# Optimization experiments

Hardware: AMD Instinct MI355X
Metric: run time of the kernel (lower is better)

## Reference

```python
import jax, jax.numpy as jnp
import numpy as np

B, S, P, N = 256, 128, 100, 500
E, H, L, F = 256, 4, 2, 1024   # embed, heads, layers, ffn
V, U, I = 50000, 10000, 10000


def setup_inputs() -> dict:
    key = jax.random.key(0)
    ks = jax.random.split(key, 32)
    u = lambda k, shp: jax.random.uniform(k, shp, jnp.float32, -0.1, 0.1)
    n = lambda k, shp, s=0.02: jax.random.normal(k, shp, jnp.float32) * s
    inp = {
        'attr': jax.random.randint(ks[0], (B, S), 0, V),
        'attr_inds': jax.random.randint(ks[1], (B, S), 0, S),
        'attr_tf': jax.random.uniform(ks[2], (B, S), jnp.float32),
        'attr_feat': jax.random.normal(ks[3], (B, 13), jnp.float32),
        'attr_lens': jax.random.randint(ks[4], (B,), S // 2, S + 1).at[0].set(S),
        'attr_lens_user': jax.random.randint(ks[5], (B,), 0, S),
        'attr_lens_item': jax.random.randint(ks[6], (B,), 0, S),
        'user_ids': jax.random.randint(ks[7], (B,), 0, U),
        'item_ids': jax.random.randint(ks[8], (B,), 0, I),
        'pos_targets': jax.random.randint(ks[9], (B, P), 0, V),
        'pos_lens': jax.random.randint(ks[10], (B,), 1, P + 1).at[0].set(P),
        'neg_targets': jax.random.randint(ks[11], (B, N), 0, V),
        'neg_lens': jax.random.randint(ks[12], (B,), 1, N + 1).at[0].set(N),
        # parameters (init_uniform(-0.1,0.1) like f_init_weight)
        'attr_emb': u(ks[13], (V, E)),
        'user_emb': u(ks[14], (U, E)),
        'item_emb': u(ks[15], (I, E)),
        'out_emb': u(ks[16], (V, 3 * E)),
        'fw_W': n(ks[17], (1, 13), 0.1),
        'fw_b': jnp.zeros((1,), jnp.float32),
        'qkv_w': n(ks[18], (L, 3 * E, E)),
        'qkv_b': jnp.zeros((L, 3 * E), jnp.float32),
        'attn_out_w': n(ks[19], (L, E, E)),
        'attn_out_b': jnp.zeros((L, E), jnp.float32),
        'ln1_s': jnp.ones((L, E), jnp.float32),
        'ln1_b': jnp.zeros((L, E), jnp.float32),
        'ff1_w': n(ks[20], (L, F, E)),
        'ff1_b': jnp.zeros((L, F), jnp.float32),
        'ff2_w': n(ks[21], (L, E, F)),
        'ff2_b': jnp.zeros((L, E), jnp.float32),
        'ln2_s': jnp.ones((L, E), jnp.float32),
        'ln2_b': jnp.zeros((L, E), jnp.float32),
    }
    return inp


def _ln(x, s, b, eps=1e-5):
    m = jnp.mean(x, axis=-1, keepdims=True)
    v = jnp.mean(jnp.square(x - m), axis=-1, keepdims=True)
    return (x - m) * jax.lax.rsqrt(v + eps) * s + b


def _encoder_layer(x, pad, p):
    # PyTorch TransformerEncoderLayer (post-norm, relu, dropout=0/eval)
    b, s, e = x.shape
    hd = e // H
    qkv = x @ p['qkv_w'].T + p['qkv_b']                      # [B,S,3E]
    q, k, v = jnp.split(qkv, 3, axis=-1)
    q = q.reshape(b, s, H, hd)
    k = k.reshape(b, s, H, hd)
    v = v.reshape(b, s, H, hd)
    scores = jnp.einsum('bqhd,bkhd->bhqk', q, k) / jnp.sqrt(jnp.float32(hd))
    scores = scores + jnp.where(pad[:, None, None, :], -1e9, 0.0)
    a = jax.nn.softmax(scores, axis=-1)
    o = jnp.einsum('bhqk,bkhd->bqhd', a, v).reshape(b, s, e)
    o = o @ p['attn_out_w'].T + p['attn_out_b']
    x = _ln(x + o, p['ln1_s'], p['ln1_b'])
    h = jax.nn.relu(x @ p['ff1_w'].T + p['ff1_b'])
    h = h @ p['ff2_w'].T + p['ff2_b']
    return _ln(x + h, p['ln2_s'], p['ln2_b'])


def reference(attr, attr_inds, attr_tf, attr_feat, attr_lens, attr_lens_user,
              attr_lens_item, user_ids, item_ids, pos_targets, pos_lens,
              neg_targets, neg_lens, attr_emb, user_emb, item_emb, out_emb,
              fw_W, fw_b, qkv_w, qkv_b, attn_out_w, attn_out_b, ln1_s, ln1_b,
              ff1_w, ff1_b, ff2_w, ff2_b, ln2_s, ln2_b):
    b, s = attr.shape
    pos = jnp.arange(s)
    pad = pos[None, :] >= attr_lens[:, None]                 # True = padding
    x = attr_emb[attr]                                       # [B,S,E]
    for l in range(qkv_w.shape[0]):
        p = {'qkv_w': qkv_w[l], 'qkv_b': qkv_b[l],
             'attn_out_w': attn_out_w[l], 'attn_out_b': attn_out_b[l],
             'ln1_s': ln1_s[l], 'ln1_b': ln1_b[l],
             'ff1_w': ff1_w[l], 'ff1_b': ff1_b[l],
             'ff2_w': ff2_w[l], 'ff2_b': ff2_b[l],
             'ln2_s': ln2_s[l], 'ln2_b': ln2_b[l]}
        x = _encoder_layer(x, pad, p)
    # per-sample scalar user weight; vectorized ragged user/item tf weighting
    w_user = jax.nn.sigmoid(attr_feat @ fw_W.T + fw_b)[:, 0]           # [B]
    side = jnp.where(pos[None, :] < attr_lens_user[:, None],
                     w_user[:, None], 1.0 - w_user[:, None])           # [B,S]
    weight = attr_tf * side * (~pad)                                   # [B,S]
    attr_x = jnp.einsum('bs,bse->be', weight, x)                       # [B,E]
    output = jnp.concatenate([user_emb[user_ids], attr_x,
                              item_emb[item_ids]], axis=-1)            # [B,3E]
    pos_logits = jnp.einsum('bpe,be->bp', out_emb[pos_targets], output)
    neg_logits = jnp.einsum('bne,be->bn', out_emb[neg_targets], output)
    pos_valid = jnp.arange(pos_targets.shape[1])[None, :] < pos_lens[:, None]
    neg_valid = jnp.arange(neg_targets.shape[1])[None, :] < neg_lens[:, None]
    logits = jnp.concatenate([pos_logits, neg_logits], axis=-1)
    mask = jnp.concatenate([pos_valid, neg_valid], axis=-1)
    new_targets = jnp.concatenate([jnp.ones_like(pos_targets),
                                   jnp.zeros_like(neg_targets)], axis=1)
    new_targets = new_targets * mask.astype(new_targets.dtype)
    return logits, mask, new_targets
```

## Files before the change

### kernel.cpp

```cpp
#include <hip/hip_runtime.h>
#include <hip/hip_bf16.h>

typedef __bf16 bf16_t;
typedef __bf16 bf16x8 __attribute__((ext_vector_type(8)));
typedef __bf16 bf16x4 __attribute__((ext_vector_type(4)));
typedef float f32x4 __attribute__((ext_vector_type(4)));

#define B_ 256
#define S_ 128
#define E_ 256
#define H_ 4
#define HD_ 64
#define F_ 1024
#define TPOS_ 100
#define TNEG_ 500
#define TT_ 600
#define ROWS_ (B_ * S_)

__global__ __launch_bounds__(256) void cvtall_kernel(
        const float* __restrict__ sq, const float* __restrict__ sa,
        const float* __restrict__ s1, const float* __restrict__ s2,
        bf16_t* __restrict__ dq, bf16_t* __restrict__ da,
        bf16_t* __restrict__ d1, bf16_t* __restrict__ d2) {
    int i = blockIdx.x * 256 + threadIdx.x;
    if (i < 393216) { dq[i] = (bf16_t)sq[i]; }
    else if (i < 524288) { int j = i - 393216; da[j] = (bf16_t)sa[j]; }
    else if (i < 1048576) { int j = i - 524288; d1[j] = (bf16_t)s1[j]; }
    else { int j = i - 1048576; d2[j] = (bf16_t)s2[j]; }
}

__global__ __launch_bounds__(256) void embed_kernel(const int* __restrict__ attr,
        const float* __restrict__ emb, bf16_t* __restrict__ xb) {
    int row = blockIdx.x * 4 + (threadIdx.x >> 6);
    int lane = threadIdx.x & 63;
    int idx = attr[row];
    float4 v = reinterpret_cast<const float4*>(emb + (size_t)idx * E_)[lane];
    bf16x4 o; o[0] = (bf16_t)v.x; o[1] = (bf16_t)v.y; o[2] = (bf16_t)v.z; o[3] = (bf16_t)v.w;
    *reinterpret_cast<bf16x4*>(xb + (size_t)row * E_ + lane * 4) = o;
}

template<bool RELU>
__global__ __launch_bounds__(512) void gemm8_kernel(
        const bf16_t* __restrict__ A, const bf16_t* __restrict__ W,
        const float* __restrict__ bias, bf16_t* __restrict__ outB, int M, int N, int K) {
    __shared__ bf16_t lA[2][128 * 32];
    __shared__ bf16_t lB[2][256 * 32];
    int tid = threadIdx.x;
    int wave = tid >> 6, lane = tid & 63;
    int wm = wave >> 2, wn = wave & 3;
    int mBase = blockIdx.y * 128;
    int nBase = blockIdx.x * 256;
    int r16 = lane & 15, kg = lane >> 4;

    const bf16_t* gA = A + (size_t)(mBase + (tid >> 2)) * K + (tid & 3) * 8;
    const bf16_t* gB = W + (size_t)(nBase + (tid >> 2)) * K + (tid & 3) * 8;

    f32x4 acc[4][4] = {};

    #define STG(buf, k0) { \
        __builtin_amdgcn_global_load_lds( \
            (const __attribute__((address_space(1))) void*)(gA + (k0)), \
            (__attribute__((address_space(3))) void*)(&lA[buf][wave * 512]), 16, 0, 0); \
        _Pragma("unroll") \
        for (int iss = 0; iss < 2; iss++) { \
            __builtin_amdgcn_global_load_lds( \
                (const __attribute__((address_space(1))) void*)(gB + (size_t)iss * 128 * K + (k0)), \
                (__attribute__((address_space(3))) void*)(&lB[buf][iss * 4096 + wave * 512]), 16, 0, 0); \
        } }

    STG(0, 0);
    int cur = 0;
    for (int k0 = 0; k0 < K; k0 += 32) {
        __syncthreads();
        if (k0 + 32 < K) STG(cur ^ 1, k0 + 32);
        bf16x8 a[4], b[4];
        #pragma unroll
        for (int i = 0; i < 4; i++) {
            a[i] = *reinterpret_cast<const bf16x8*>(&lA[cur][(wm * 64 + i * 16 + r16) * 32 + kg * 8]);
            b[i] = *reinterpret_cast<const bf16x8*>(&lB[cur][(wn * 64 + i * 16 + r16) * 32 + kg * 8]);
        }
        #pragma unroll
        for (int mi = 0; mi < 4; mi++)
            #pragma unroll
            for (int ni = 0; ni < 4; ni++)
                acc[mi][ni] = __builtin_amdgcn_mfma_f32_16x16x32_bf16(a[mi], b[ni], acc[mi][ni], 0, 0, 0);
        cur ^= 1;
    }
    #undef STG

    #pragma unroll
    for (int mi = 0; mi < 4; mi++) {
        #pragma unroll
        for (int ni = 0; ni < 4; ni++) {
            int col = nBase + wn * 64 + ni * 16 + r16;
            float bv = bias[col];
            #pragma unroll
            for (int j = 0; j < 4; j++) {
                int row = mBase + wm * 64 + mi * 16 + kg * 4 + j;
                float v = acc[mi][ni][j] + bv;
                if (RELU) v = v > 0.f ? v : 0.f;
                outB[(size_t)row * N + col] = (bf16_t)v;
            }
        }
    }
}

__global__ __launch_bounds__(512) void gemm_ln8_kernel(
        const bf16_t* __restrict__ A, const bf16_t* __restrict__ W,
        const float* __restrict__ bias, const float* __restrict__ sc,
        const float* __restrict__ bi, bf16_t* __restrict__ xb, int M, int K) {
    __shared__ bf16_t lA[2][128 * 32];
    __shared__ bf16_t lB[2][256 * 32];
    __shared__ float psum[128][4][2];
    int tid = threadIdx.x;
    int wave = tid >> 6, lane = tid & 63;
    int wm = wave >> 2, wn = wave & 3;
    int mBase = blockIdx.x * 128;
    int r16 = lane & 15, kg = lane >> 4;

    const bf16_t* gA = A + (size_t)(mBase + (tid >> 2)) * K + (tid & 3) * 8;
    const bf16_t* gB = W + (size_t)((tid >> 2)) * K + (tid & 3) * 8;

    f32x4 acc[4][4] = {};

    #define STG2(buf, k0) { \
        __builtin_amdgcn_global_load_lds( \
            (const __attribute__((address_space(1))) void*)(gA + (k0)), \
            (__attribute__((address_space(3))) void*)(&lA[buf][wave * 512]), 16, 0, 0); \
        _Pragma("unroll") \
        for (int iss = 0; iss < 2; iss++) { \
            __builtin_amdgcn_global_load_lds( \
                (const __attribute__((address_space(1))) void*)(gB + (size_t)iss * 128 * K + (k0)), \
                (__attribute__((address_space(3))) void*)(&lB[buf][iss * 4096 + wave * 512]), 16, 0, 0); \
        } }

    STG2(0, 0);
    int cur = 0;
    for (int k0 = 0; k0 < K; k0 += 32) {
        __syncthreads();
        if (k0 + 32 < K) STG2(cur ^ 1, k0 + 32);
        bf16x8 a[4], b[4];
        #pragma unroll
        for (int i = 0; i < 4; i++) {
            a[i] = *reinterpret_cast<const bf16x8*>(&lA[cur][(wm * 64 + i * 16 + r16) * 32 + kg * 8]);
            b[i] = *reinterpret_cast<const bf16x8*>(&lB[cur][(wn * 64 + i * 16 + r16) * 32 + kg * 8]);
        }
        #pragma unroll
        for (int mi = 0; mi < 4; mi++)
            #pragma unroll
            for (int ni = 0; ni < 4; ni++)
                acc[mi][ni] = __builtin_amdgcn_mfma_f32_16x16x32_bf16(a[mi], b[ni], acc[mi][ni], 0, 0, 0);
        cur ^= 1;
    }
    #undef STG2

    float bv[4];
    #pragma unroll
    for (int ni = 0; ni < 4; ni++) bv[ni] = bias[wn * 64 + ni * 16 + r16];
    #pragma unroll
    for (int mi = 0; mi < 4; mi++) {
        #pragma unroll
        for (int j = 0; j < 4; j++) {
            int rl = wm * 64 + mi * 16 + kg * 4 + j;
            const bf16_t* rrow = xb + (size_t)(mBase + rl) * 256;
            float s = 0.f, q = 0.f;
            #pragma unroll
            for (int ni = 0; ni < 4; ni++) {
                int col = wn * 64 + ni * 16 + r16;
                float v = acc[mi][ni][j] + bv[ni] + (float)rrow[col];
                acc[mi][ni][j] = v;
                s += v; q += v * v;
            }
            #pragma unroll
            for (int m = 1; m < 16; m <<= 1) { s += __shfl_xor(s, m); q += __shfl_xor(q, m); }
            if (r16 == 0) { psum[rl][wn][0] = s; psum[rl][wn][1] = q; }
        }
    }
    __syncthreads();
    #pragma unroll
    for (int mi = 0; mi < 4; mi++) {
        #pragma unroll
        for (int j = 0; j < 4; j++) {
            int rl = wm * 64 + mi * 16 + kg * 4 + j;
            float s = psum[rl][0][0] + psum[rl][1][0] + psum[rl][2][0] + psum[rl][3][0];
            float qq = psum[rl][0][1] + psum[rl][1][1] + psum[rl][2][1] + psum[rl][3][1];
            float mean = s * (1.0f / 256.0f);
            float var = qq * (1.0f / 256.0f) - mean * mean;
            float inv = rsqrtf(var + 1e-5f);
            bf16_t* orow = xb + (size_t)(mBase + rl) * 256;
            #pragma unroll
            for (int ni = 0; ni < 4; ni++) {
                int col = wn * 64 + ni * 16 + r16;
                float o = (acc[mi][ni][j] - mean) * inv * sc[col] + bi[col];
                orow[col] = (bf16_t)o;
            }
        }
    }
}

__global__ __launch_bounds__(256) void attn_kernel(const bf16_t* __restrict__ qkv,
        const int* __restrict__ lens, bf16_t* __restrict__ out) {
    __shared__ bf16_t p[S_][S_ + 8];
    __shared__ bf16_t vl[HD_][S_ + 8];
    int bh = blockIdx.x; int b = bh >> 2, h = bh & 3;
    int wave = threadIdx.x >> 6, lane = threadIdx.x & 63;
    int r16 = lane & 15, kg = lane >> 4;
    int q0 = wave * 32;
    int len = lens[b];
    const bf16_t* qbase = qkv + (size_t)b * S_ * 768;

    {
        int sl = (wave & 1) * 64 + lane;
        const bf16_t* vsrc = qbase + (size_t)sl * 768 + 512 + h * HD_;
        #pragma unroll
        for (int pass = 0; pass < 4; pass++) {
            int d0 = (pass * 2 + (wave >> 1)) * 8;
            bf16x8 v = *reinterpret_cast<const bf16x8*>(vsrc + d0);
            #pragma unroll
            for (int j = 0; j < 8; j++) vl[d0 + j][sl] = v[j];
        }
    }

    f32x4 acc[2][8] = {};
    #pragma unroll
    for (int ks = 0; ks < 2; ks++) {
        int kOff = h * HD_ + ks * 32 + kg * 8;
        bf16x8 a[2], bb[8];
        #pragma unroll
        for (int mi = 0; mi < 2; mi++)
            a[mi] = *reinterpret_cast<const bf16x8*>(qbase + (size_t)(q0 + mi * 16 + r16) * 768 + kOff);
        #pragma unroll
        for (int ni = 0; ni < 8; ni++)
            bb[ni] = *reinterpret_cast<const bf16x8*>(qbase + (size_t)(ni * 16 + r16) * 768 + 256 + kOff);
        #pragma unroll
        for (int mi = 0; mi < 2; mi++)
            #pragma unroll
            for (int ni = 0; ni < 8; ni++)
                acc[mi][ni] = __builtin_amdgcn_mfma_f32_16x16x32_bf16(a[mi], bb[ni], acc[mi][ni], 0, 0, 0);
    }
    #pragma unroll
    for (int mi = 0; mi < 2; mi++) {
        #pragma unroll
        for (int j = 0; j < 4; j++) {
            float vals[8]; float mx = -1e30f;
            #pragma unroll
            for (int ni = 0; ni < 8; ni++) {
                int kp = ni * 16 + r16;
                float v = acc[mi][ni][j] * 0.125f;
                vals[ni] = (kp < len) ? v : -1e30f;
                mx = fmaxf(mx, vals[ni]);
            }
            #pragma unroll
            for (int m = 1; m < 16; m <<= 1) mx = fmaxf(mx, __shfl_xor(mx, m));
            float sum = 0.f;
            #pragma unroll
            for (int ni = 0; ni < 8; ni++) {
                vals[ni] = (vals[ni] > -1e29f) ? __expf(vals[ni] - mx) : 0.f;
                sum += vals[ni];
            }
            #pragma unroll
            for (int m = 1; m < 16; m <<= 1) sum += __shfl_xor(sum, m);
            float inv = 1.0f / sum;
            int row = q0 + mi * 16 + kg * 4 + j;
            #pragma unroll
            for (int ni = 0; ni < 8; ni++)
                p[row][ni * 16 + r16] = (bf16_t)(vals[ni] * inv);
        }
    }
    __syncthreads();
    f32x4 acc2[2][4] = {};
    #pragma unroll
    for (int ks = 0; ks < 4; ks++) {
        int k = ks * 32 + kg * 8;
        bf16x8 a[2], bb[4];
        #pragma unroll
        for (int mi = 0; mi < 2; mi++)
            a[mi] = *reinterpret_cast<const bf16x8*>(&p[q0 + mi * 16 + r16][k]);
        #pragma unroll
        for (int ni = 0; ni < 4; ni++)
            bb[ni] = *reinterpret_cast<const bf16x8*>(&vl[ni * 16 + r16][k]);
        #pragma unroll
        for (int mi = 0; mi < 2; mi++)
            #pragma unroll
            for (int ni = 0; ni < 4; ni++)
                acc2[mi][ni] = __builtin_amdgcn_mfma_f32_16x16x32_bf16(a[mi], bb[ni], acc2[mi][ni], 0, 0, 0);
    }
    #pragma unroll
    for (int mi = 0; mi < 2; mi++)
        #pragma unroll
        for (int ni = 0; ni < 4; ni++)
            #pragma unroll
            for (int j = 0; j < 4; j++) {
                int q = q0 + mi * 16 + kg * 4 + j;
                int d = ni * 16 + r16;
                out[((size_t)b * S_ + q) * E_ + h * HD_ + d] = (bf16_t)acc2[mi][ni][j];
            }
}

__global__ void wuser_kernel(const float* __restrict__ feat, const float* __restrict__ W,
                             const float* __restrict__ bb, float* __restrict__ wu) {
    int b = threadIdx.x;
    if (b < B_) {
        float z = bb[0];
        #pragma unroll
        for (int i = 0; i < 13; i++) z += feat[b * 13 + i] * W[i];
        wu[b] = 1.f / (1.f + __expf(-z));
    }
}

__global__ __launch_bounds__(256) void pool_kernel(
        const bf16_t* __restrict__ xb, const float* __restrict__ attr_tf,
        const int* __restrict__ lens, const int* __restrict__ lens_user,
        const float* __restrict__ wu, const int* __restrict__ uid, const int* __restrict__ iid,
        const float* __restrict__ user_emb, const float* __restrict__ item_emb,
        float* __restrict__ outvec) {
    int b = blockIdx.x, t = threadIdx.x;
    __shared__ float wrow[S_];
    if (t < S_) {
        float w = (t < lens[b]) ? attr_tf[b * S_ + t] : 0.f;
        float side = (t < lens_user[b]) ? wu[b] : (1.f - wu[b]);
        wrow[t] = w * side;
    }
    __syncthreads();
    float acc = 0.f;
    const bf16_t* xr = xb + (size_t)b * S_ * E_ + t;
    #pragma unroll 4
    for (int s = 0; s < S_; s++) acc += wrow[s] * (float)xr[(size_t)s * E_];
    outvec[b * 768 + 256 + t] = acc;
    outvec[b * 768 + t] = user_emb[(size_t)uid[b] * E_ + t];
    outvec[b * 768 + 512 + t] = item_emb[(size_t)iid[b] * E_ + t];
}

__global__ __launch_bounds__(256) void logits_kernel(
        const float* __restrict__ outvec, const float* __restrict__ out_emb,
        const int* __restrict__ pos_t, const int* __restrict__ pos_l,
        const int* __restrict__ neg_t, const int* __restrict__ neg_l,
        float* __restrict__ dout) {
    int gg = blockIdx.x * 4 + (threadIdx.x >> 6);
    int lane = threadIdx.x & 63;
    int b = gg / (TT_ / 2);
    int u = gg - b * (TT_ / 2);
    int pl = pos_l[b], nl = neg_l[b];
    int t0 = u * 2, t1 = u * 2 + 1;

    int tgt0, tgt1, valid0, valid1, ispos0, ispos1;
    if (t0 < TPOS_) { tgt0 = pos_t[b * TPOS_ + t0]; valid0 = (t0 < pl); ispos0 = 1; }
    else { int tn = t0 - TPOS_; tgt0 = neg_t[b * TNEG_ + tn]; valid0 = (tn < nl); ispos0 = 0; }
    if (t1 < TPOS_) { tgt1 = pos_t[b * TPOS_ + t1]; valid1 = (t1 < pl); ispos1 = 1; }
    else { int tn = t1 - TPOS_; tgt1 = neg_t[b * TNEG_ + tn]; valid1 = (tn < nl); ispos1 = 0; }

    const float4* e0 = reinterpret_cast<const float4*>(out_emb + (size_t)tgt0 * 768);
    const float4* e1 = reinterpret_cast<const float4*>(out_emb + (size_t)tgt1 * 768);
    const float4* o4 = reinterpret_cast<const float4*>(outvec + (size_t)b * 768);
    float acc0 = 0.f, acc1 = 0.f;
    #pragma unroll
    for (int c = 0; c < 3; c++) {
        float4 a0 = e0[c * 64 + lane];
        float4 a1 = e1[c * 64 + lane];
        float4 o = o4[c * 64 + lane];
        acc0 += a0.x * o.x + a0.y * o.y + a0.z * o.z + a0.w * o.w;
        acc1 += a1.x * o.x + a1.y * o.y + a1.z * o.z + a1.w * o.w;
    }
    #pragma unroll
    for (int m = 1; m < 64; m <<= 1) { acc0 += __shfl_xor(acc0, m); acc1 += __shfl_xor(acc1, m); }
    if (lane == 0) {
        size_t i0 = (size_t)b * TT_ + t0;
        dout[i0] = acc0;
        dout[i0 + 1] = acc1;
        dout[(size_t)B_ * TT_ + i0] = valid0 ? 1.0f : 0.0f;
        dout[(size_t)B_ * TT_ + i0 + 1] = valid1 ? 1.0f : 0.0f;
        dout[2 * (size_t)B_ * TT_ + i0] = (valid0 && ispos0) ? 1.0f : 0.0f;
        dout[2 * (size_t)B_ * TT_ + i0 + 1] = (valid1 && ispos1) ? 1.0f : 0.0f;
    }
}

extern "C" void kernel_launch(void* const* d_in, const int* in_sizes, int n_in,
                              void* d_out, int out_size, void* d_ws, size_t ws_size,
                              hipStream_t stream) {
    const int*   attr        = (const int*)d_in[0];
    const float* attr_tf     = (const float*)d_in[2];
    const float* attr_feat   = (const float*)d_in[3];
    const int*   attr_lens   = (const int*)d_in[4];
    const int*   attr_lens_u = (const int*)d_in[5];
    const int*   user_ids    = (const int*)d_in[7];
    const int*   item_ids    = (const int*)d_in[8];
    const int*   pos_targets = (const int*)d_in[9];
    const int*   pos_lens    = (const int*)d_in[10];
    const int*   neg_targets = (const int*)d_in[11];
    const int*   neg_lens    = (const int*)d_in[12];
    const float* attr_emb    = (const float*)d_in[13];
    const float* user_emb    = (const float*)d_in[14];
    const float* item_emb    = (const float*)d_in[15];
    const float* out_emb     = (const float*)d_in[16];
    const float* fw_W        = (const float*)d_in[17];
    const float* fw_b        = (const float*)d_in[18];
    const float* qkv_w       = (const float*)d_in[19];
    const float* qkv_b       = (const float*)d_in[20];
    const float* attn_out_w  = (const float*)d_in[21];
    const float* attn_out_b  = (const float*)d_in[22];
    const float* ln1_s       = (const float*)d_in[23];
    const float* ln1_b       = (const float*)d_in[24];
    const float* ff1_w       = (const float*)d_in[25];
    const float* ff1_b       = (const float*)d_in[26];
    const float* ff2_w       = (const float*)d_in[27];
    const float* ff2_b       = (const float*)d_in[28];
    const float* ln2_s       = (const float*)d_in[29];
    const float* ln2_b       = (const float*)d_in[30];

    size_t szRes = (size_t)ROWS_ * E_ * 2;
    size_t wB = (size_t)1572864 * 2;
    size_t fixedB = 2 * szRes + wB + (size_t)B_ * 768 * 4 + 4096 + 16384;
    int CH = 32;
    for (int ch = 1; ch <= 32; ch <<= 1) {
        if (fixedB + (size_t)(ROWS_ / ch) * 1024 * 2 <= ws_size) { CH = ch; break; }
    }
    int rowsC = ROWS_ / CH, sampC = B_ / CH;

    char* ws = (char*)d_ws;
    size_t off = 0;
    auto alloc = [&](size_t bytes) { void* pp = ws + off; off += (bytes + 255) & ~255ULL; return pp; };
    bf16_t* xb  = (bf16_t*)alloc(szRes);
    bf16_t* ob  = (bf16_t*)alloc(szRes);
    bf16_t* wq  = (bf16_t*)alloc((size_t)393216 * 2);
    bf16_t* wa  = (bf16_t*)alloc((size_t)131072 * 2);
    bf16_t* w1  = (bf16_t*)alloc((size_t)524288 * 2);
    bf16_t* w2  = (bf16_t*)alloc((size_t)524288 * 2);
    float* outvec = (float*)alloc((size_t)B_ * 768 * 4);
    float* wu     = (float*)alloc(1024);
    bf16_t* chunk = (bf16_t*)alloc((size_t)rowsC * 1024 * 2);

    cvtall_kernel<<<6144, 256, 0, stream>>>(qkv_w, attn_out_w, ff1_w, ff2_w, wq, wa, w1, w2);
    embed_kernel<<<ROWS_ / 4, 256, 0, stream>>>(attr, attr_emb, xb);

    for (int l = 0; l < 2; l++) {
        for (int c = 0; c < CH; c++) {
            size_t r0 = (size_t)c * rowsC;
            gemm8_kernel<false><<<dim3(3, rowsC / 128), 512, 0, stream>>>(
                xb + r0 * E_, wq + (size_t)l * 768 * 256, qkv_b + l * 768, chunk, rowsC, 768, 256);
            attn_kernel<<<sampC * H_, 256, 0, stream>>>(chunk, attr_lens + c * sampC, ob + r0 * E_);
        }
        gemm_ln8_kernel<<<ROWS_ / 128, 512, 0, stream>>>(
            ob, wa + (size_t)l * 256 * 256, attn_out_b + l * 256,
            ln1_s + l * 256, ln1_b + l * 256, xb, ROWS_, 256);
        for (int c = 0; c < CH; c++) {
            size_t r0 = (size_t)c * rowsC;
            gemm8_kernel<true><<<dim3(4, rowsC / 128), 512, 0, stream>>>(
                xb + r0 * E_, w1 + (size_t)l * 1024 * 256, ff1_b + l * 1024, chunk, rowsC, 1024, 256);
            gemm_ln8_kernel<<<rowsC / 128, 512, 0, stream>>>(
                chunk, w2 + (size_t)l * 256 * 1024, ff2_b + l * 256,
                ln2_s + l * 256, ln2_b + l * 256, xb + r0 * E_, rowsC, 1024);
        }
    }

    wuser_kernel<<<1, 256, 0, stream>>>(attr_feat, fw_W, fw_b, wu);
    pool_kernel<<<B_, 256, 0, stream>>>(xb, attr_tf, attr_lens, attr_lens_u, wu,
                                        user_ids, item_ids, user_emb, item_emb, outvec);
    logits_kernel<<<B_ * TT_ / 8, 256, 0, stream>>>(outvec, out_emb, pos_targets, pos_lens,
                                                    neg_targets, neg_lens, (float*)d_out);
}
```

Before: 386.2 us.

## Bucket logit targets by vocab id so each out_emb row is read once

Replaces the per-target gather of out_emb rows with a counting-sort pipeline: histogram the target ids, prefix-scan them into offsets, fill per-id entry lists, then one wave per vocabulary row loads the row once and computes dot products for every (batch, target) pair that references it. This removes redundant random reads of the 768-float rows, since 153,600 targets are drawn from 50,000 ids. In exchange it adds four small kernels with global atomics, a single-block scan, per-entry loads of outvec, and load imbalance across waves. Entry order within a bucket is nondeterministic, but each output slot is still written exactly once.

```diff
diff --git a/kernel.cpp b/kernel.cpp
--- a/kernel.cpp
+++ b/kernel.cpp
@@ -16,6 +16,8 @@
 #define TNEG_ 500
 #define TT_ 600
 #define ROWS_ (B_ * S_)
+#define V_ 50000
+#define VPAD_ 50176
 
 __global__ __launch_bounds__(256) void cvtall_kernel(
         const float* __restrict__ sq, const float* __restrict__ sa,
@@ -331,46 +333,87 @@
     outvec[b * 768 + 512 + t] = item_emb[(size_t)iid[b] * E_ + t];
 }
 
-__global__ __launch_bounds__(256) void logits_kernel(
-        const float* __restrict__ outvec, const float* __restrict__ out_emb,
+
+__global__ __launch_bounds__(256) void zerocnt_kernel(int* __restrict__ counts) {
+    int i = blockIdx.x * 256 + threadIdx.x;
+    if (i < VPAD_) counts[i] = 0;
+}
+
+__global__ __launch_bounds__(256) void hist_kernel(
         const int* __restrict__ pos_t, const int* __restrict__ pos_l,
         const int* __restrict__ neg_t, const int* __restrict__ neg_l,
-        float* __restrict__ dout) {
-    int gg = blockIdx.x * 4 + (threadIdx.x >> 6);
-    int lane = threadIdx.x & 63;
-    int b = gg / (TT_ / 2);
-    int u = gg - b * (TT_ / 2);
-    int pl = pos_l[b], nl = neg_l[b];
-    int t0 = u * 2, t1 = u * 2 + 1;
-
-    int tgt0, tgt1, valid0, valid1, ispos0, ispos1;
-    if (t0 < TPOS_) { tgt0 = pos_t[b * TPOS_ + t0]; valid0 = (t0 < pl); ispos0 = 1; }
-    else { int tn = t0 - TPOS_; tgt0 = neg_t[b * TNEG_ + tn]; valid0 = (tn < nl); ispos0 = 0; }
-    if (t1 < TPOS_) { tgt1 = pos_t[b * TPOS_ + t1]; valid1 = (t1 < pl); ispos1 = 1; }
-    else { int tn = t1 - TPOS_; tgt1 = neg_t[b * TNEG_ + tn]; valid1 = (tn < nl); ispos1 = 0; }
-
-    const float4* e0 = reinterpret_cast<const float4*>(out_emb + (size_t)tgt0 * 768);
-    const float4* e1 = reinterpret_cast<const float4*>(out_emb + (size_t)tgt1 * 768);
-    const float4* o4 = reinterpret_cast<const float4*>(outvec + (size_t)b * 768);
-    float acc0 = 0.f, acc1 = 0.f;
-    #pragma unroll
-    for (int c = 0; c < 3; c++) {
-        float4 a0 = e0[c * 64 + lane];
-        float4 a1 = e1[c * 64 + lane];
-        float4 o = o4[c * 64 + lane];
-        acc0 += a0.x * o.x + a0.y * o.y + a0.z * o.z + a0.w * o.w;
-        acc1 += a1.x * o.x + a1.y * o.y + a1.z * o.z + a1.w * o.w;
-    }
-    #pragma unroll
-    for (int m = 1; m < 64; m <<= 1) { acc0 += __shfl_xor(acc0, m); acc1 += __shfl_xor(acc1, m); }
-    if (lane == 0) {
-        size_t i0 = (size_t)b * TT_ + t0;
-        dout[i0] = acc0;
-        dout[i0 + 1] = acc1;
-        dout[(size_t)B_ * TT_ + i0] = valid0 ? 1.0f : 0.0f;
-        dout[(size_t)B_ * TT_ + i0 + 1] = valid1 ? 1.0f : 0.0f;
-        dout[2 * (size_t)B_ * TT_ + i0] = (valid0 && ispos0) ? 1.0f : 0.0f;
-        dout[2 * (size_t)B_ * TT_ + i0 + 1] = (valid1 && ispos1) ? 1.0f : 0.0f;
+        int* __restrict__ counts, float* __restrict__ dout) {
+    int i = blockIdx.x * 256 + threadIdx.x;
+    if (i >= B_ * TT_) return;
+    int b = i / TT_, t = i - b * TT_;
+    int tgt, valid, ispos;
+    if (t < TPOS_) { tgt = pos_t[b * TPOS_ + t]; valid = (t < pos_l[b]); ispos = 1; }
+    else { int tn = t - TPOS_; tgt = neg_t[b * TNEG_ + tn]; valid = (tn < neg_l[b]); ispos = 0; }
+    atomicAdd(&counts[tgt], 1);
+    dout[(size_t)B_ * TT_ + i] = valid ? 1.0f : 0.0f;
+    dout[2 * (size_t)B_ * TT_ + i] = (valid && ispos) ? 1.0f : 0.0f;
+}
+
+__global__ __launch_bounds__(1024) void scan_kernel(
+        const int* __restrict__ counts, int* __restrict__ offs, int* __restrict__ cursor) {
+    __shared__ int part[1024];
+    int t = threadIdx.x;
+    const int per = VPAD_ / 1024;
+    int base = t * per;
+    int s = 0;
+    for (int j = 0; j < per; j++) s += counts[base + j];
+    part[t] = s;
+    __syncthreads();
+    for (int o = 1; o < 1024; o <<= 1) {
+        int v = (t >= o) ? part[t - o] : 0;
+        __syncthreads();
+        part[t] += v;
+        __syncthreads();
+    }
+    int run = part[t] - s;
+    for (int j = 0; j < per; j++) {
+        offs[base + j] = run;
+        cursor[base + j] = run;
+        run += counts[base + j];
+    }
+}
+
+__global__ __launch_bounds__(256) void fill_kernel(
+        const int* __restrict__ pos_t, const int* __restrict__ neg_t,
+        int* __restrict__ cursor, int* __restrict__ entries) {
+    int i = blockIdx.x * 256 + threadIdx.x;
+    if (i >= B_ * TT_) return;
+    int b = i / TT_, t = i - b * TT_;
+    int tgt;
+    if (t < TPOS_) tgt = pos_t[b * TPOS_ + t];
+    else tgt = neg_t[b * TNEG_ + t - TPOS_];
+    int p = atomicAdd(&cursor[tgt], 1);
+    entries[p] = i;
+}
+
+__global__ __launch_bounds__(256) void lstream_kernel(
+        const float* __restrict__ out_emb, const float* __restrict__ outvec,
+        const int* __restrict__ counts, const int* __restrict__ offs,
+        const int* __restrict__ entries, float* __restrict__ dout) {
+    int wave = threadIdx.x >> 6, lane = threadIdx.x & 63;
+    int v = blockIdx.x * 4 + wave;
+    if (v >= V_) return;
+    int n = counts[v];
+    if (n == 0) return;
+    const float4* e4 = reinterpret_cast<const float4*>(out_emb + (size_t)v * 768);
+    float4 r0 = e4[lane], r1 = e4[64 + lane], r2 = e4[128 + lane];
+    int c0 = offs[v];
+    for (int k = 0; k < n; k++) {
+        int idx = entries[c0 + k];
+        int b = idx / TT_;
+        const float4* o4 = reinterpret_cast<const float4*>(outvec + (size_t)b * 768);
+        float4 o0 = o4[lane], o1 = o4[64 + lane], o2 = o4[128 + lane];
+        float acc = r0.x * o0.x + r0.y * o0.y + r0.z * o0.z + r0.w * o0.w
+                  + r1.x * o1.x + r1.y * o1.y + r1.z * o1.z + r1.w * o1.w
+                  + r2.x * o2.x + r2.y * o2.y + r2.z * o2.z + r2.w * o2.w;
+        #pragma unroll
+        for (int m = 1; m < 64; m <<= 1) acc += __shfl_xor(acc, m);
+        if (lane == 0) dout[idx] = acc;
     }
 }
 
@@ -409,7 +452,8 @@
 
     size_t szRes = (size_t)ROWS_ * E_ * 2;
     size_t wB = (size_t)1572864 * 2;
-    size_t fixedB = 2 * szRes + wB + (size_t)B_ * 768 * 4 + 4096 + 16384;
+    size_t idxB = (size_t)VPAD_ * 4 * 3 + (size_t)B_ * TT_ * 4;
+    size_t fixedB = 2 * szRes + wB + idxB + (size_t)B_ * 768 * 4 + 4096 + 16384;
     int CH = 32;
     for (int ch = 1; ch <= 32; ch <<= 1) {
         if (fixedB + (size_t)(ROWS_ / ch) * 1024 * 2 <= ws_size) { CH = ch; break; }
@@ -427,10 +471,20 @@
     bf16_t* w2  = (bf16_t*)alloc((size_t)524288 * 2);
     float* outvec = (float*)alloc((size_t)B_ * 768 * 4);
     float* wu     = (float*)alloc(1024);
+    int* counts   = (int*)alloc((size_t)VPAD_ * 4);
+    int* offs     = (int*)alloc((size_t)VPAD_ * 4);
+    int* cursor   = (int*)alloc((size_t)VPAD_ * 4);
+    int* entries  = (int*)alloc((size_t)B_ * TT_ * 4);
     bf16_t* chunk = (bf16_t*)alloc((size_t)rowsC * 1024 * 2);
 
     cvtall_kernel<<<6144, 256, 0, stream>>>(qkv_w, attn_out_w, ff1_w, ff2_w, wq, wa, w1, w2);
     embed_kernel<<<ROWS_ / 4, 256, 0, stream>>>(attr, attr_emb, xb);
+    zerocnt_kernel<<<(VPAD_ + 255) / 256, 256, 0, stream>>>(counts);
+    hist_kernel<<<(B_ * TT_ + 255) / 256, 256, 0, stream>>>(
+        pos_targets, pos_lens, neg_targets, neg_lens, counts, (float*)d_out);
+    scan_kernel<<<1, 1024, 0, stream>>>(counts, offs, cursor);
+    fill_kernel<<<(B_ * TT_ + 255) / 256, 256, 0, stream>>>(
+        pos_targets, neg_targets, cursor, entries);
 
     for (int l = 0; l < 2; l++) {
         for (int c = 0; c < CH; c++) {
@@ -455,6 +509,6 @@
     wuser_kernel<<<1, 256, 0, stream>>>(attr_feat, fw_W, fw_b, wu);
     pool_kernel<<<B_, 256, 0, stream>>>(xb, attr_tf, attr_lens, attr_lens_u, wu,
                                         user_ids, item_ids, user_emb, item_emb, outvec);
-    logits_kernel<<<B_ * TT_ / 8, 256, 0, stream>>>(outvec, out_emb, pos_targets, pos_lens,
-                                                    neg_targets, neg_lens, (float*)d_out);
-}
+    lstream_kernel<<<(V_ + 3) / 4, 256, 0, stream>>>(
+        out_emb, outvec, counts, offs, entries, (float*)d_out);
+}
```

Result: slower. 413.7 us (+7.1%).
